# Kernel tuning notes

Hardware: AMD Instinct MI355X
Metric: run time of the kernel (lower is better)

The kernel has to match this reference:

```python
import jax, jax.numpy as jnp
import numpy as np

HIDDEN = 2048
NUM_HEADS = 16
HEAD_DIM = 128
KV_C = 512
Q_C = 1536
ROPE_DIM = 64
B, S = 2, 2048


def _rope(x):
    # x: [B, H, S, D] with D even; interleaved-pair rotation as in the torch module
    b, h, s, d = x.shape
    inv_freq = 1.0 / (10000.0 ** (jnp.arange(0, d, 2, dtype=jnp.float32) / d))  # [d/2]
    pos = jnp.arange(s, dtype=jnp.float32)
    sinusoid = pos[:, None] * inv_freq[None, :]  # [S, d/2]
    sin, cos = jnp.sin(sinusoid), jnp.cos(sinusoid)
    xr = x.reshape(b, h, s, d // 2, 2)
    x1, x2 = xr[..., 0], xr[..., 1]
    out = jnp.stack([x1 * cos - x2 * sin, x1 * sin + x2 * cos], axis=-1)
    return out.reshape(b, h, s, d)


def setup_inputs() -> dict:
    key = jax.random.key(0)
    ks = jax.random.split(key, 12)

    def lin(k, fan_in, fan_out):
        k1, k2 = jax.random.split(k)
        lim = 1.0 / np.sqrt(fan_in)
        w = jax.random.uniform(k1, (fan_in, fan_out), jnp.float32, -lim, lim)
        b = jax.random.uniform(k2, (fan_out,), jnp.float32, -lim, lim)
        return w, b

    kv_down_w, kv_down_b = lin(ks[0], HIDDEN, KV_C)
    key_up_w, key_up_b = lin(ks[1], KV_C, NUM_HEADS * HEAD_DIM)
    value_up_w, value_up_b = lin(ks[2], KV_C, NUM_HEADS * HEAD_DIM)
    key_rope_w, key_rope_b = lin(ks[3], KV_C, NUM_HEADS * ROPE_DIM)
    query_down_w, query_down_b = lin(ks[4], HIDDEN, Q_C)
    query_up_w, query_up_b = lin(ks[5], Q_C, NUM_HEADS * HEAD_DIM)
    query_rope_w, query_rope_b = lin(ks[6], Q_C, NUM_HEADS * ROPE_DIM)
    out_w, out_b = lin(ks[7], NUM_HEADS * HEAD_DIM, HIDDEN)

    x = jax.random.normal(ks[8], (B, S, HIDDEN), jnp.float32)
    attention_mask = jnp.ones((B, S), dtype=jnp.bool_)  # all tokens valid

    return dict(x=x, attention_mask=attention_mask,
                kv_down_w=kv_down_w, kv_down_b=kv_down_b,
                key_up_w=key_up_w, key_up_b=key_up_b,
                value_up_w=value_up_w, value_up_b=value_up_b,
                key_rope_w=key_rope_w, key_rope_b=key_rope_b,
                query_down_w=query_down_w, query_down_b=query_down_b,
                query_up_w=query_up_w, query_up_b=query_up_b,
                query_rope_w=query_rope_w, query_rope_b=query_rope_b,
                out_w=out_w, out_b=out_b)


def reference(x, attention_mask,
              kv_down_w, kv_down_b, key_up_w, key_up_b,
              value_up_w, value_up_b, key_rope_w, key_rope_b,
              query_down_w, query_down_b, query_up_w, query_up_b,
              query_rope_w, query_rope_b, out_w, out_b):
    b, s, _ = x.shape

    kv_c = x @ kv_down_w + kv_down_b                                 # [B,S,KV_C]
    keys_c = (kv_c @ key_up_w + key_up_b).reshape(b, s, NUM_HEADS, HEAD_DIM).transpose(0, 2, 1, 3)
    values = (kv_c @ value_up_w + value_up_b).reshape(b, s, NUM_HEADS, HEAD_DIM).transpose(0, 2, 1, 3)
    keys_r = (kv_c @ key_rope_w + key_rope_b).reshape(b, s, NUM_HEADS, ROPE_DIM).transpose(0, 2, 1, 3)
    keys_r = _rope(keys_r)

    q_c = x @ query_down_w + query_down_b                            # [B,S,Q_C]
    queries_c = (q_c @ query_up_w + query_up_b).reshape(b, s, NUM_HEADS, HEAD_DIM).transpose(0, 2, 1, 3)
    queries_r = (q_c @ query_rope_w + query_rope_b).reshape(b, s, NUM_HEADS, ROPE_DIM).transpose(0, 2, 1, 3)
    queries_r = _rope(queries_r)

    queries = jnp.concatenate([queries_c, queries_r], axis=-1)      # [B,H,S,HD+RD]
    keys = jnp.concatenate([keys_c, keys_r], axis=-1)

    scale = 1.0 / np.sqrt(HEAD_DIM + ROPE_DIM)
    scores = jnp.einsum('bhqd,bhkd->bhqk', queries, keys) * scale   # [B,H,S,S]

    causal = jnp.triu(jnp.ones((s, s), dtype=jnp.bool_), k=1)       # True = masked
    pad = ~attention_mask                                            # [B,S], True = masked key
    mask = causal[None, None, :, :] | pad[:, None, None, :]
    scores = jnp.where(mask, jnp.float32(-1e9), scores)

    probs = jax.nn.softmax(scores, axis=-1)
    context = jnp.einsum('bhqk,bhkd->bhqd', probs, values)          # [B,H,S,HD]
    context = context.transpose(0, 2, 1, 3).reshape(b, s, NUM_HEADS * HEAD_DIM)
    return context @ out_w + out_b                                   # [B,S,HIDDEN]
```

## Files before the change

### kernel.cpp

```cpp
#include <hip/hip_runtime.h>

typedef unsigned short u16;
typedef short short8 __attribute__((ext_vector_type(8)));
typedef short short4v __attribute__((ext_vector_type(4)));
typedef float floatx4 __attribute__((ext_vector_type(4)));
typedef float floatx4v __attribute__((ext_vector_type(4)));

#define SQ 2048
#define NH 16
#define HD 128
#define RD 64
#define NB 2
#define LDKV 5120
#define LDQ 3072

#define LKC 136
#define LKR 72
#define LVT 72
#define LP  72

__device__ __forceinline__ float bf2f(u16 u) {
  union { unsigned u; float f; } v; v.u = ((unsigned)u) << 16; return v.f;
}
__device__ __forceinline__ u16 f2bf(float f) {
  union { float f; unsigned u; } v; v.f = f;
  return (u16)((v.u + 0x7FFFu + ((v.u >> 16) & 1u)) >> 16);
}
__device__ __forceinline__ void gll16(const u16* g, u16* l) {
  __builtin_amdgcn_global_load_lds((const __attribute__((address_space(1))) void*)g,
                                   (__attribute__((address_space(3))) void*)l, 16, 0, 0);
}

__global__ __launch_bounds__(256) void convert_x(const float* __restrict__ src,
                                                 u16* __restrict__ dst, int n4) {
  const int i = blockIdx.x * 256 + threadIdx.x;
  if (i >= n4) return;
  const floatx4v v = *(const floatx4v*)(src + 4 * (size_t)i);
  short4v o;
  o.x = (short)f2bf(v.x); o.y = (short)f2bf(v.y);
  o.z = (short)f2bf(v.z); o.w = (short)f2bf(v.w);
  *(short4v*)(dst + 4 * (size_t)i) = o;
}

__global__ __launch_bounds__(256) void convert_biases(
    const float* b0, const float* b1, const float* b2, const float* b3,
    const float* b4, const float* b5, const float* b6, const float* b7,
    u16* __restrict__ bc) {
  const int i = blockIdx.x * 256 + threadIdx.x;
  if (i >= 12288) return;
  float v;
  if      (i < 512)   v = b0[i];
  else if (i < 2048)  v = b1[i - 512];
  else if (i < 4096)  v = b2[i - 2048];
  else if (i < 6144)  v = b3[i - 4096];
  else if (i < 7168)  v = b4[i - 6144];
  else if (i < 9216)  v = b5[i - 7168];
  else if (i < 10240) v = b6[i - 9216];
  else                v = b7[i - 10240];
  bc[i] = f2bf(v);
}

__global__ __launch_bounds__(256) void transpose_w(const float* __restrict__ in,
                                                   u16* __restrict__ out,
                                                   int R, int C) {
  __shared__ u16 tile[32][33];
  const int c0 = blockIdx.x * 32, r0 = blockIdx.y * 32;
  const int x = threadIdx.x & 31, y = threadIdx.x >> 5;
#pragma unroll
  for (int i = 0; i < 32; i += 8)
    tile[y + i][x] = f2bf(in[(size_t)(r0 + y + i) * C + c0 + x]);
  __syncthreads();
#pragma unroll
  for (int i = 0; i < 32; i += 8)
    out[(size_t)(c0 + y + i) * R + r0 + x] = tile[x][y + i];
}

__global__ __launch_bounds__(256) void transpose_v(const u16* __restrict__ KV,
                                                   u16* __restrict__ Vt) {
  __shared__ u16 tile[32][33];
  const int bh = blockIdx.z, b = bh >> 4, hh = bh & 15;
  const u16* pin = KV + (size_t)b * SQ * LDKV + 2048 + (size_t)hh * HD;
  u16* pout = Vt + (size_t)bh * HD * SQ;
  const int s0 = blockIdx.x * 32, d0 = blockIdx.y * 32;
  const int x = threadIdx.x & 31, y = threadIdx.x >> 5;
#pragma unroll
  for (int i = 0; i < 32; i += 8)
    tile[y + i][x] = pin[(size_t)(s0 + y + i) * LDKV + d0 + x];
  __syncthreads();
#pragma unroll
  for (int i = 0; i < 32; i += 8)
    pout[(size_t)(d0 + y + i) * SQ + s0 + x] = tile[x][y + i];
}

__global__ __launch_bounds__(256) void rope_inplace(u16* __restrict__ buf,
                                                    int ld, int coloff) {
  const int i = blockIdx.x * 256 + threadIdx.x;
  if (i >= NB * SQ * NH * 32) return;
  const int j = i & 31;
  const int hh = (i >> 5) & 15;
  const int row = i >> 9;
  const int s = row & (SQ - 1);
  u16* p = buf + (size_t)row * ld + coloff + hh * RD + 2 * j;
  const float x1 = bf2f(p[0]), x2 = bf2f(p[1]);
  const float inv = exp2f(-(float)j * 0.41524101186092031f);
  const float ang = (float)s * inv;
  float sn, cs;
  sincosf(ang, &sn, &cs);
  p[0] = f2bf(x1 * cs - x2 * sn);
  p[1] = f2bf(x1 * sn + x2 * cs);
}

__global__ __launch_bounds__(256) void gemm_bt(const u16* __restrict__ A, int lda,
                                               const u16* __restrict__ Bt,
                                               const u16* __restrict__ bias,
                                               void* __restrict__ Cout, int ldc,
                                               int wf32, int N, int K) {
  __shared__ __align__(16) u16 lA[2][128 * 32];
  __shared__ __align__(16) u16 lB[2][128 * 32];
  const int t = threadIdx.x;
  const int lane = t & 63, w = t >> 6;
  const int wm = w & 1, wn = w >> 1;
  const int gx = gridDim.x;
  const int nwg = gx * gridDim.y;
  const int bid = blockIdx.y * gx + blockIdx.x;
  const int cpx = nwg >> 3;
  const int sbid = (bid & 7) * cpx + (bid >> 3);
  const int m0 = (sbid / gx) * 128, n0 = (sbid % gx) * 128;
  const int srow = t >> 2, scol = (t & 3) * 8;
  const u16* gA = A + (size_t)(m0 + srow) * lda + scol;
  const u16* gB = Bt + (size_t)(n0 + srow) * K + scol;
  const int lane_m = lane & 15, lane_k = (lane >> 4) * 8;

  auto stage = [&](int b, int k0) {
    gll16(gA + k0, lA[b] + (16 * w) * 32);
    gll16(gA + (size_t)64 * lda + k0, lA[b] + (64 + 16 * w) * 32);
    gll16(gB + k0, lB[b] + (16 * w) * 32);
    gll16(gB + (size_t)64 * K + k0, lB[b] + (64 + 16 * w) * 32);
  };

  floatx4 acc[4][4] = {};
  stage(0, 0);
  __syncthreads();
  int cur = 0;
  for (int k0 = 0; k0 < K; k0 += 32) {
    if (k0 + 32 < K) stage(cur ^ 1, k0 + 32);
    short8 af[4], bf[4];
#pragma unroll
    for (int i = 0; i < 4; i++)
      af[i] = *(const short8*)(lA[cur] + (wm * 64 + i * 16 + lane_m) * 32 + lane_k);
#pragma unroll
    for (int i = 0; i < 4; i++)
      bf[i] = *(const short8*)(lB[cur] + (wn * 64 + i * 16 + lane_m) * 32 + lane_k);
#pragma unroll
    for (int mi = 0; mi < 4; mi++)
#pragma unroll
      for (int ni = 0; ni < 4; ni++)
        acc[mi][ni] = __builtin_amdgcn_mfma_f32_16x16x32_bf16(af[mi], bf[ni], acc[mi][ni], 0, 0, 0);
    __syncthreads();
    cur ^= 1;
  }
  const int quad = lane >> 4;
#pragma unroll
  for (int ni = 0; ni < 4; ni++) {
    const int col = n0 + wn * 64 + ni * 16 + lane_m;
    const float bv = bf2f(bias[col]);
#pragma unroll
    for (int mi = 0; mi < 4; mi++) {
      const int row = m0 + wm * 64 + mi * 16 + quad * 4;
      if (wf32) {
        float* pc = (float*)Cout + (size_t)row * ldc + col;
#pragma unroll
        for (int r = 0; r < 4; r++)
          pc[(size_t)r * ldc] = acc[mi][ni][r] + bv;
      } else {
        u16* pc = (u16*)Cout + (size_t)row * ldc + col;
#pragma unroll
        for (int r = 0; r < 4; r++)
          pc[(size_t)r * ldc] = f2bf(acc[mi][ni][r] + bv);
      }
    }
  }
}

__global__ __launch_bounds__(512, 4) void flash_attn(const u16* __restrict__ Q,
                                                     const u16* __restrict__ KV,
                                                     const u16* __restrict__ Vt,
                                                     u16* __restrict__ Ctx) {
  __shared__ __align__(16) u16 lKc[64 * LKC];
  __shared__ __align__(16) u16 lKr[64 * LKR];
  __shared__ __align__(16) u16 lVt[128 * LVT];
  __shared__ __align__(16) u16 lP[8 * 16 * LP];
  const int t = threadIdx.x, lane = t & 63, w = t >> 6;
  const int col = blockIdx.y;
  const int qtile = (col < 16) ? (15 - (int)blockIdx.x) : (int)blockIdx.x;
  const int h = col & (NH - 1);
  const int b = col >> 4;
  const int q0 = qtile * 128;
  const int nkt = 2 * qtile + 2;
  const int lane_m = lane & 15, quad = lane >> 4, lane_k = quad * 8;

  const int qrow = q0 + 16 * w + lane_m;
  const u16* qcp = Q + (size_t)(b * SQ + qrow) * LDQ + h * HD;
  const u16* qrp = Q + (size_t)(b * SQ + qrow) * LDQ + 2048 + h * RD;
  short8 qfc[4], qfr[2];
#pragma unroll
  for (int ks = 0; ks < 4; ks++) qfc[ks] = *(const short8*)(qcp + ks * 32 + lane_k);
#pragma unroll
  for (int ks = 0; ks < 2; ks++) qfr[ks] = *(const short8*)(qrp + ks * 32 + lane_k);

  floatx4 O[8] = {};
  float mrow[4], lsum[4];
#pragma unroll
  for (int r = 0; r < 4; r++) { mrow[r] = -1e30f; lsum[r] = 0.f; }

  const u16* gKc = KV + (size_t)b * SQ * LDKV + h * HD;
  const u16* gKr = KV + (size_t)b * SQ * LDKV + 4096 + h * RD;
  const u16* gVt = Vt + (size_t)(b * NH + h) * HD * SQ;
  const float C2 = 0.10412825525540364f;
  const float THR = 28.8f;

  short8 rKc[2], rKr, rVt[2];
  auto load_tile = [&](int kb) {
#pragma unroll
    for (int i = 0; i < 2; i++) {
      const int c = t + i * 512, row = c >> 4, cc = (c & 15) * 8;
      rKc[i] = *(const short8*)(gKc + (size_t)(kb + row) * LDKV + cc);
    }
    {
      const int row = t >> 3, cc = (t & 7) * 8;
      rKr = *(const short8*)(gKr + (size_t)(kb + row) * LDKV + cc);
    }
#pragma unroll
    for (int i = 0; i < 2; i++) {
      const int c = t + i * 512, row = c >> 3, cc = (c & 7) * 8;
      rVt[i] = *(const short8*)(gVt + (size_t)row * SQ + kb + cc);
    }
  };

  const int wrow_lo = q0 + 16 * w;
  const int wrow_hi = wrow_lo + 15;

  load_tile(0);
  for (int kt = 0; kt < nkt; kt++) {
    const int kb = kt * 64;
    __syncthreads();
#pragma unroll
    for (int i = 0; i < 2; i++) {
      const int c = t + i * 512, row = c >> 4, cc = (c & 15) * 8;
      *(short8*)(lKc + row * LKC + cc) = rKc[i];
    }
    {
      const int row = t >> 3, cc = (t & 7) * 8;
      *(short8*)(lKr + row * LKR + cc) = rKr;
    }
#pragma unroll
    for (int i = 0; i < 2; i++) {
      const int c = t + i * 512, row = c >> 3, cc = (c & 7) * 8;
      *(short8*)(lVt + row * LVT + cc) = rVt[i];
    }
    __syncthreads();
    if (kt < nkt - 1) load_tile(kb + 64);

    if (kb <= wrow_hi) {
      float ss[4][4];
      __builtin_amdgcn_s_setprio(1);
#pragma unroll
      for (int n = 0; n < 4; n++) {
        floatx4 a = {0.f, 0.f, 0.f, 0.f};
#pragma unroll
        for (int ks = 0; ks < 4; ks++) {
          const short8 kf = *(const short8*)(lKc + (n * 16 + lane_m) * LKC + ks * 32 + lane_k);
          a = __builtin_amdgcn_mfma_f32_16x16x32_bf16(qfc[ks], kf, a, 0, 0, 0);
        }
#pragma unroll
        for (int ks = 0; ks < 2; ks++) {
          const short8 kf = *(const short8*)(lKr + (n * 16 + lane_m) * LKR + ks * 32 + lane_k);
          a = __builtin_amdgcn_mfma_f32_16x16x32_bf16(qfr[ks], kf, a, 0, 0, 0);
        }
#pragma unroll
        for (int r = 0; r < 4; r++) ss[n][r] = a[r];
      }
      __builtin_amdgcn_s_setprio(0);
      if (kb + 63 > wrow_lo) {
#pragma unroll
        for (int n = 0; n < 4; n++) {
          const int kcol = kb + n * 16 + lane_m;
#pragma unroll
          for (int r = 0; r < 4; r++) {
            const int row = wrow_lo + quad * 4 + r;
            if (kcol > row) ss[n][r] = -1e30f;
          }
        }
      }
      float mt[4];
#pragma unroll
      for (int r = 0; r < 4; r++) {
        float m = fmaxf(fmaxf(ss[0][r], ss[1][r]), fmaxf(ss[2][r], ss[3][r]));
#pragma unroll
        for (int d = 1; d < 16; d <<= 1) m = fmaxf(m, __shfl_xor(m, d));
        mt[r] = m;
      }
      const bool grow = (mt[0] > mrow[0] + THR) || (mt[1] > mrow[1] + THR) ||
                        (mt[2] > mrow[2] + THR) || (mt[3] > mrow[3] + THR);
      if (__any(grow)) {
#pragma unroll
        for (int r = 0; r < 4; r++) {
          const float mn = fmaxf(mrow[r], mt[r]);
          const float alpha = exp2f((mrow[r] - mn) * C2);
          mrow[r] = mn;
          lsum[r] *= alpha;
#pragma unroll
          for (int vb = 0; vb < 8; vb++) O[vb][r] *= alpha;
        }
      }
      float pw[4][4];
#pragma unroll
      for (int r = 0; r < 4; r++) {
        float s = 0.f;
#pragma unroll
        for (int n = 0; n < 4; n++) {
          const float p = exp2f((ss[n][r] - mrow[r]) * C2);
          pw[n][r] = p;
          s += p;
        }
#pragma unroll
        for (int d = 1; d < 16; d <<= 1) s += __shfl_xor(s, d);
        lsum[r] += s;
      }
#pragma unroll
      for (int n = 0; n < 4; n++)
#pragma unroll
        for (int r = 0; r < 4; r++)
          lP[(w * 16 + quad * 4 + r) * LP + n * 16 + lane_m] = f2bf(pw[n][r]);
      asm volatile("s_waitcnt lgkmcnt(0)" ::: "memory");
      __builtin_amdgcn_s_setprio(1);
#pragma unroll
      for (int ks = 0; ks < 2; ks++) {
        const short8 pf = *(const short8*)(lP + (w * 16 + lane_m) * LP + ks * 32 + lane_k);
#pragma unroll
        for (int vb = 0; vb < 8; vb++) {
          const short8 vf = *(const short8*)(lVt + (vb * 16 + lane_m) * LVT + ks * 32 + lane_k);
          O[vb] = __builtin_amdgcn_mfma_f32_16x16x32_bf16(pf, vf, O[vb], 0, 0, 0);
        }
      }
      __builtin_amdgcn_s_setprio(0);
    }
  }
  float inv[4];
#pragma unroll
  for (int r = 0; r < 4; r++) inv[r] = 1.f / lsum[r];
#pragma unroll
  for (int vb = 0; vb < 8; vb++) {
#pragma unroll
    for (int r = 0; r < 4; r++) {
      const int row = wrow_lo + quad * 4 + r;
      Ctx[(size_t)(b * SQ + row) * 2048 + h * HD + vb * 16 + lane_m] = f2bf(O[vb][r] * inv[r]);
    }
  }
}

extern "C" void kernel_launch(void* const* d_in, const int* in_sizes, int n_in,
                              void* d_out, int out_size, void* d_ws, size_t ws_size,
                              hipStream_t stream) {
  (void)in_sizes; (void)n_in; (void)out_size; (void)ws_size;
  const float* x    = (const float*)d_in[0];
  const float* kvdw = (const float*)d_in[2];
  const float* kvdb = (const float*)d_in[3];
  const float* kuw  = (const float*)d_in[4];
  const float* kub  = (const float*)d_in[5];
  const float* vuw  = (const float*)d_in[6];
  const float* vub  = (const float*)d_in[7];
  const float* krw  = (const float*)d_in[8];
  const float* krb  = (const float*)d_in[9];
  const float* qdw  = (const float*)d_in[10];
  const float* qdb  = (const float*)d_in[11];
  const float* quw  = (const float*)d_in[12];
  const float* qub  = (const float*)d_in[13];
  const float* qrw  = (const float*)d_in[14];
  const float* qrb  = (const float*)d_in[15];
  const float* ow   = (const float*)d_in[16];
  const float* ob   = (const float*)d_in[17];

  u16* p = (u16*)d_ws;
  u16* bc   = p;  p += 16384;
  u16* WT1  = p;  p += (size_t)2048 * 2048;
  u16* WT2  = p;  p += (size_t)5120 * 512;
  u16* WT3  = p;  p += (size_t)3072 * 1536;
  u16* Ctx  = WT1;
  u16* WTo  = p;  p += (size_t)2048 * 2048;
  u16* KVQd = p;  p += (size_t)4096 * 2048;
  u16* Vt   = KVQd;
  u16* KV   = p;  p += (size_t)4096 * 5120;
  u16* Qb   = p;  p += (size_t)4096 * 3072;
  u16* xc   = Qb;

  convert_x<<<dim3(8192), 256, 0, stream>>>(x, xc, 4096 * 2048 / 4);
  convert_biases<<<dim3(48), 256, 0, stream>>>(kvdb, qdb, kub, vub, krb, qub, qrb, ob, bc);

  auto T = [&](const float* in, u16* out, int R, int C) {
    transpose_w<<<dim3(C / 32, R / 32), 256, 0, stream>>>(in, out, R, C);
  };
  T(kvdw, WT1, 2048, 512);
  T(qdw,  WT1 + (size_t)512 * 2048, 2048, 1536);
  T(kuw,  WT2, 512, 2048);
  T(vuw,  WT2 + (size_t)2048 * 512, 512, 2048);
  T(krw,  WT2 + (size_t)4096 * 512, 512, 1024);
  T(quw,  WT3, 1536, 2048);
  T(qrw,  WT3 + (size_t)2048 * 1536, 1536, 1024);
  T(ow,   WTo, 2048, 2048);

  auto G = [&](const u16* A, int lda, const u16* Bt, const u16* bias,
               void* Cout, int ldc, int wf32, int N, int K) {
    gemm_bt<<<dim3(N / 128, 4096 / 128), 256, 0, stream>>>(A, lda, Bt, bias, Cout, ldc, wf32, N, K);
  };
  G(xc, 2048, WT1, bc, KVQd, 2048, 0, 2048, 2048);
  G(KVQd, 2048, WT2, bc + 2048, KV, LDKV, 0, 5120, 512);
  G(KVQd + 512, 2048, WT3, bc + 7168, Qb, LDQ, 0, 3072, 1536);

  rope_inplace<<<dim3((NB * SQ * NH * 32) / 256), 256, 0, stream>>>(KV, LDKV, 4096);
  rope_inplace<<<dim3((NB * SQ * NH * 32) / 256), 256, 0, stream>>>(Qb, LDQ, 2048);
  transpose_v<<<dim3(SQ / 32, HD / 32, NB * NH), 256, 0, stream>>>(KV, Vt);
  flash_attn<<<dim3(16, 32), 512, 0, stream>>>(Qb, KV, Vt, Ctx);

  G(Ctx, 2048, WTo, bc + 10240, d_out, 2048, 1, 2048, 2048);
}
```

Baseline: 536.0 us.

## Restructure GEMM to 512 threads with K=64 steps, drop swizzle and prefetch

The GEMM now runs 8 waves per block, each owning a 64x32 subtile, and loads two K=32 slabs per iteration into separate LDS buffers before one barrier. The old double-buffered prefetch that overlapped global loads with MFMA is gone, so each iteration waits on its loads. The XCD-aware block remapping is also replaced by plain blockIdx mapping. The aim is fewer barriers per K and more waves to hide latency, at the cost of losing load/compute overlap and L2 locality across chiplets. Staging is consistent with the new thread count: 512 threads times 16 bytes cover each 128x32 tile once.

```diff
diff --git a/kernel.cpp b/kernel.cpp
--- a/kernel.cpp
+++ b/kernel.cpp
@@ -110,59 +110,68 @@
   p[1] = f2bf(x1 * sn + x2 * cs);
 }
 
-__global__ __launch_bounds__(256) void gemm_bt(const u16* __restrict__ A, int lda,
-                                               const u16* __restrict__ Bt,
-                                               const u16* __restrict__ bias,
-                                               void* __restrict__ Cout, int ldc,
-                                               int wf32, int N, int K) {
-  __shared__ __align__(16) u16 lA[2][128 * 32];
-  __shared__ __align__(16) u16 lB[2][128 * 32];
+__global__ __launch_bounds__(512, 4) void gemm_bt(const u16* __restrict__ A, int lda,
+                                                  const u16* __restrict__ Bt,
+                                                  const u16* __restrict__ bias,
+                                                  void* __restrict__ Cout, int ldc,
+                                                  int wf32, int N, int K) {
+  __shared__ __align__(16) u16 lAk0[128 * 32];
+  __shared__ __align__(16) u16 lAk1[128 * 32];
+  __shared__ __align__(16) u16 lBk0[128 * 32];
+  __shared__ __align__(16) u16 lBk1[128 * 32];
   const int t = threadIdx.x;
   const int lane = t & 63, w = t >> 6;
   const int wm = w & 1, wn = w >> 1;
-  const int gx = gridDim.x;
-  const int nwg = gx * gridDim.y;
-  const int bid = blockIdx.y * gx + blockIdx.x;
-  const int cpx = nwg >> 3;
-  const int sbid = (bid & 7) * cpx + (bid >> 3);
-  const int m0 = (sbid / gx) * 128, n0 = (sbid % gx) * 128;
+  const int m0 = blockIdx.y * 128, n0 = blockIdx.x * 128;
   const int srow = t >> 2, scol = (t & 3) * 8;
   const u16* gA = A + (size_t)(m0 + srow) * lda + scol;
   const u16* gB = Bt + (size_t)(n0 + srow) * K + scol;
+  u16* const ldA0 = lAk0 + (16 * w) * 32;
+  u16* const ldA1 = lAk1 + (16 * w) * 32;
+  u16* const ldB0 = lBk0 + (16 * w) * 32;
+  u16* const ldB1 = lBk1 + (16 * w) * 32;
   const int lane_m = lane & 15, lane_k = (lane >> 4) * 8;
-
-  auto stage = [&](int b, int k0) {
-    gll16(gA + k0, lA[b] + (16 * w) * 32);
-    gll16(gA + (size_t)64 * lda + k0, lA[b] + (64 + 16 * w) * 32);
-    gll16(gB + k0, lB[b] + (16 * w) * 32);
-    gll16(gB + (size_t)64 * K + k0, lB[b] + (64 + 16 * w) * 32);
-  };
-
-  floatx4 acc[4][4] = {};
-  stage(0, 0);
-  __syncthreads();
-  int cur = 0;
-  for (int k0 = 0; k0 < K; k0 += 32) {
-    if (k0 + 32 < K) stage(cur ^ 1, k0 + 32);
-    short8 af[4], bf[4];
-#pragma unroll
-    for (int i = 0; i < 4; i++)
-      af[i] = *(const short8*)(lA[cur] + (wm * 64 + i * 16 + lane_m) * 32 + lane_k);
-#pragma unroll
-    for (int i = 0; i < 4; i++)
-      bf[i] = *(const short8*)(lB[cur] + (wn * 64 + i * 16 + lane_m) * 32 + lane_k);
-#pragma unroll
-    for (int mi = 0; mi < 4; mi++)
-#pragma unroll
-      for (int ni = 0; ni < 4; ni++)
-        acc[mi][ni] = __builtin_amdgcn_mfma_f32_16x16x32_bf16(af[mi], bf[ni], acc[mi][ni], 0, 0, 0);
+  floatx4 acc[4][2] = {};
+  for (int k0 = 0; k0 < K; k0 += 64) {
+    gll16(gA + k0, ldA0);
+    gll16(gA + k0 + 32, ldA1);
+    gll16(gB + k0, ldB0);
+    gll16(gB + k0 + 32, ldB1);
     __syncthreads();
-    cur ^= 1;
+    {
+      short8 af[4], bf[2];
+#pragma unroll
+      for (int i = 0; i < 4; i++)
+        af[i] = *(const short8*)(lAk0 + (wm * 64 + i * 16 + lane_m) * 32 + lane_k);
+#pragma unroll
+      for (int i = 0; i < 2; i++)
+        bf[i] = *(const short8*)(lBk0 + (wn * 32 + i * 16 + lane_m) * 32 + lane_k);
+#pragma unroll
+      for (int mi = 0; mi < 4; mi++)
+#pragma unroll
+        for (int ni = 0; ni < 2; ni++)
+          acc[mi][ni] = __builtin_amdgcn_mfma_f32_16x16x32_bf16(af[mi], bf[ni], acc[mi][ni], 0, 0, 0);
+    }
+    {
+      short8 af[4], bf[2];
+#pragma unroll
+      for (int i = 0; i < 4; i++)
+        af[i] = *(const short8*)(lAk1 + (wm * 64 + i * 16 + lane_m) * 32 + lane_k);
+#pragma unroll
+      for (int i = 0; i < 2; i++)
+        bf[i] = *(const short8*)(lBk1 + (wn * 32 + i * 16 + lane_m) * 32 + lane_k);
+#pragma unroll
+      for (int mi = 0; mi < 4; mi++)
+#pragma unroll
+        for (int ni = 0; ni < 2; ni++)
+          acc[mi][ni] = __builtin_amdgcn_mfma_f32_16x16x32_bf16(af[mi], bf[ni], acc[mi][ni], 0, 0, 0);
+    }
+    __syncthreads();
   }
   const int quad = lane >> 4;
 #pragma unroll
-  for (int ni = 0; ni < 4; ni++) {
-    const int col = n0 + wn * 64 + ni * 16 + lane_m;
+  for (int ni = 0; ni < 2; ni++) {
+    const int col = n0 + wn * 32 + ni * 16 + lane_m;
     const float bv = bf2f(bias[col]);
 #pragma unroll
     for (int mi = 0; mi < 4; mi++) {
@@ -411,7 +420,7 @@
 
   auto G = [&](const u16* A, int lda, const u16* Bt, const u16* bias,
                void* Cout, int ldc, int wf32, int N, int K) {
-    gemm_bt<<<dim3(N / 128, 4096 / 128), 256, 0, stream>>>(A, lda, Bt, bias, Cout, ldc, wf32, N, K);
+    gemm_bt<<<dim3(N / 128, 4096 / 128), 512, 0, stream>>>(A, lda, Bt, bias, Cout, ldc, wf32, N, K);
   };
   G(xc, 2048, WT1, bc, KVQd, 2048, 0, 2048, 2048);
   G(KVQd, 2048, WT2, bc + 2048, KV, LDKV, 0, 5120, 512);
```

Result: faster. 523.4 us (-2.4%).
